# Optimization experiments

Measured on AMD Instinct MI355X. Metric: run time of the kernel, lower is better.

The kernel has to match this reference:

```python
import jax, jax.numpy as jnp
import numpy as np

N = 2_000_000
NUM_CLASSES = 64


def setup_inputs() -> dict:
    key = jax.random.key(0)
    k1, k2 = jax.random.split(key)
    # log-probability-like inputs (log_softmax so exp sums are well-scaled)
    logits = jax.random.normal(k1, (N, NUM_CLASSES), dtype=jnp.float32)
    predictions = jax.nn.log_softmax(logits, axis=-1)
    targets = jax.random.randint(k2, (N,), 0, NUM_CLASSES, dtype=jnp.int64)
    return {"predictions": predictions, "targets": targets}


def reference(predictions, targets):
    n = predictions.shape[0]
    num_classes = predictions.shape[1]
    # class_dist[i] = count of class i in targets  (create_distribution_tensor)
    ones = jnp.ones_like(targets, dtype=predictions.dtype)
    class_dist = jax.ops.segment_sum(ones, targets, num_segments=num_classes)
    # column sums of exp(predictions): sum_n exp(pred)[n, i]
    col_sum = jnp.sum(jnp.exp(predictions), axis=0)  # [C]
    penalty = jnp.sum((class_dist - col_sum) ** 2) / n
    # F.nll_loss with default mean reduction: -mean_n pred[n, targets[n]]
    picked = jnp.take_along_axis(predictions, targets[:, None], axis=1)[:, 0]
    nll = -jnp.mean(picked)
    return nll + penalty
```

## Files before the change

kernel.cpp:

```cpp
#include <hip/hip_runtime.h>

#define NUM_CLASSES 64
#define UNROLL 4
#define SLAB 16

typedef float f32x4 __attribute__((ext_vector_type(4)));

__global__ __launch_bounds__(256) void loss_pass1(
    const float* __restrict__ pred,
    const int* __restrict__ tgt,
    float* __restrict__ g_colsum,
    unsigned int* __restrict__ g_cnt,
    float* __restrict__ g_nll,
    int n)
{
    __shared__ float s_col[NUM_CLASSES];
    __shared__ unsigned int s_cnt[NUM_CLASSES];
    __shared__ float s_nll[4];

    const int t = threadIdx.x;
    if (t < NUM_CLASSES) { s_col[t] = 0.0f; s_cnt[t] = 0u; }
    __syncthreads();

    const int c16  = t & 15;
    const int rloc = t >> 4;
    const int c0   = c16 * 4;
    const int rows_per_block = SLAB * UNROLL;
    const long stride = (long)rows_per_block * gridDim.x;

    float ca0 = 0.f, ca1 = 0.f, ca2 = 0.f, ca3 = 0.f;
    float nllacc = 0.f;

    for (long base = (long)blockIdx.x * rows_per_block; base < n; base += stride) {
        f32x4 v[UNROLL];
        int   tg[UNROLL];

        if (base + rows_per_block <= n) {
            #pragma unroll
            for (int j = 0; j < UNROLL; ++j) {
                const long row = base + rloc + j * SLAB;
                v[j]  = __builtin_nontemporal_load(
                          reinterpret_cast<const f32x4*>(pred + row * NUM_CLASSES + c0));
                tg[j] = tgt[row];
            }
            #pragma unroll
            for (int j = 0; j < UNROLL; ++j) {
                ca0 += __expf(v[j][0]);
                ca1 += __expf(v[j][1]);
                ca2 += __expf(v[j][2]);
                ca3 += __expf(v[j][3]);
                if (c16 == j) atomicAdd(&s_cnt[tg[j]], 1u);
                const int d = tg[j] - c0;
                if ((unsigned)d < 4u) nllacc += v[j][d];
            }
        } else {
            #pragma unroll
            for (int j = 0; j < UNROLL; ++j) {
                const long row = base + rloc + j * SLAB;
                if (row >= n) continue;
                const f32x4 w = *reinterpret_cast<const f32x4*>(pred + row * NUM_CLASSES + c0);
                const int g = tgt[row];
                ca0 += __expf(w[0]);
                ca1 += __expf(w[1]);
                ca2 += __expf(w[2]);
                ca3 += __expf(w[3]);
                if (c16 == j) atomicAdd(&s_cnt[g], 1u);
                const int d = g - c0;
                if ((unsigned)d < 4u) nllacc += w[d];
            }
        }
    }

    atomicAdd(&s_col[c0 + 0], ca0);
    atomicAdd(&s_col[c0 + 1], ca1);
    atomicAdd(&s_col[c0 + 2], ca2);
    atomicAdd(&s_col[c0 + 3], ca3);

    for (int off = 32; off; off >>= 1) nllacc += __shfl_down(nllacc, off);
    if ((t & 63) == 0) s_nll[t >> 6] = nllacc;
    __syncthreads();

    if (t == 0) atomicAdd(g_nll, s_nll[0] + s_nll[1] + s_nll[2] + s_nll[3]);
    if (t < NUM_CLASSES) {
        atomicAdd(&g_colsum[t], s_col[t]);
        atomicAdd(&g_cnt[t], s_cnt[t]);
    }
}

__global__ void loss_finalize(const float* __restrict__ g_colsum,
                              const unsigned int* __restrict__ g_cnt,
                              const float* __restrict__ g_nll,
                              float* __restrict__ out, int n)
{
    const int t = threadIdx.x;
    const float diff = (float)g_cnt[t] - g_colsum[t];
    float p = diff * diff;
    for (int off = 32; off; off >>= 1) p += __shfl_down(p, off);
    if (t == 0) out[0] = (p - g_nll[0]) / (float)n;
}

extern "C" void kernel_launch(void* const* d_in, const int* in_sizes, int n_in,
                              void* d_out, int out_size, void* d_ws, size_t ws_size,
                              hipStream_t stream)
{
    const float* pred = (const float*)d_in[0];
    const int* tgt    = (const int*)d_in[1];
    const int n       = in_sizes[1];

    float*        g_colsum = (float*)d_ws;
    unsigned int* g_cnt    = (unsigned int*)((char*)d_ws + 256);
    float*        g_nll    = (float*)((char*)d_ws + 512);

    hipMemsetAsync(d_ws, 0, 1024, stream);

    loss_pass1<<<2048, 256, 0, stream>>>(pred, tgt, g_colsum, g_cnt, g_nll, n);
    loss_finalize<<<1, 64, 0, stream>>>(g_colsum, g_cnt, g_nll, (float*)d_out, n);
}
```

Measured before the change: 104.6 us.

## Replace global atomics and memset with per-block partials and parallel finalize

Each block now writes its per-class column sums, counts and NLL partial to a workspace slot instead of issuing global atomics, which also removes the hipMemsetAsync launch. A 1024-thread finalize kernel reduces the partials. Rows are split into contiguous per-block ranges rather than grid-strided slabs, and dynamic vector indexing is replaced by a select chain. This trades global atomic contention and a memset for extra workspace traffic and a heavier finalize.

```diff
diff --git a/kernel.cpp b/kernel.cpp
--- a/kernel.cpp
+++ b/kernel.cpp
@@ -1,73 +1,70 @@
 #include <hip/hip_runtime.h>
 
 #define NUM_CLASSES 64
-#define UNROLL 4
-#define SLAB 16
+#define MAX_GRID 2048
 
 typedef float f32x4 __attribute__((ext_vector_type(4)));
 
 __global__ __launch_bounds__(256) void loss_pass1(
     const float* __restrict__ pred,
     const int* __restrict__ tgt,
-    float* __restrict__ g_colsum,
-    unsigned int* __restrict__ g_cnt,
-    float* __restrict__ g_nll,
-    int n)
+    float* __restrict__ part_col,
+    float* __restrict__ part_cnt,
+    float* __restrict__ part_nll,
+    int n, int grid)
 {
     __shared__ float s_col[NUM_CLASSES];
     __shared__ unsigned int s_cnt[NUM_CLASSES];
     __shared__ float s_nll[4];
 
     const int t = threadIdx.x;
-    if (t < NUM_CLASSES) { s_col[t] = 0.0f; s_cnt[t] = 0u; }
+    if (t < NUM_CLASSES) { s_col[t] = 0.f; s_cnt[t] = 0u; }
     __syncthreads();
 
     const int c16  = t & 15;
     const int rloc = t >> 4;
     const int c0   = c16 * 4;
-    const int rows_per_block = SLAB * UNROLL;
-    const long stride = (long)rows_per_block * gridDim.x;
+
+    const long start = (long)blockIdx.x * n / grid;
+    const long end   = (long)(blockIdx.x + 1) * n / grid;
 
     float ca0 = 0.f, ca1 = 0.f, ca2 = 0.f, ca3 = 0.f;
     float nllacc = 0.f;
 
-    for (long base = (long)blockIdx.x * rows_per_block; base < n; base += stride) {
-        f32x4 v[UNROLL];
-        int   tg[UNROLL];
+    long base = start;
+    for (; base + 64 <= end; base += 64) {
+        f32x4 v[4];
+        int   tg[4];
+        #pragma unroll
+        for (int j = 0; j < 4; ++j) {
+            const long row = base + rloc + j * 16;
+            v[j]  = __builtin_nontemporal_load(
+                      reinterpret_cast<const f32x4*>(pred + row * NUM_CLASSES + c0));
+            tg[j] = tgt[row];
+        }
+        #pragma unroll
+        for (int j = 0; j < 4; ++j) {
+            ca0 += __expf(v[j][0]);
+            ca1 += __expf(v[j][1]);
+            ca2 += __expf(v[j][2]);
+            ca3 += __expf(v[j][3]);
+            if (c16 == j) atomicAdd(&s_cnt[tg[j]], 1u);
+            const int d = tg[j] - c0;
+            if ((unsigned)d < 4u)
+                nllacc += (d==0)?v[j][0]:(d==1)?v[j][1]:(d==2)?v[j][2]:v[j][3];
+        }
+    }
 
-        if (base + rows_per_block <= n) {
-            #pragma unroll
-            for (int j = 0; j < UNROLL; ++j) {
-                const long row = base + rloc + j * SLAB;
-                v[j]  = __builtin_nontemporal_load(
-                          reinterpret_cast<const f32x4*>(pred + row * NUM_CLASSES + c0));
-                tg[j] = tgt[row];
-            }
-            #pragma unroll
-            for (int j = 0; j < UNROLL; ++j) {
-                ca0 += __expf(v[j][0]);
-                ca1 += __expf(v[j][1]);
-                ca2 += __expf(v[j][2]);
-                ca3 += __expf(v[j][3]);
-                if (c16 == j) atomicAdd(&s_cnt[tg[j]], 1u);
-                const int d = tg[j] - c0;
-                if ((unsigned)d < 4u) nllacc += v[j][d];
-            }
-        } else {
-            #pragma unroll
-            for (int j = 0; j < UNROLL; ++j) {
-                const long row = base + rloc + j * SLAB;
-                if (row >= n) continue;
-                const f32x4 w = *reinterpret_cast<const f32x4*>(pred + row * NUM_CLASSES + c0);
-                const int g = tgt[row];
-                ca0 += __expf(w[0]);
-                ca1 += __expf(w[1]);
-                ca2 += __expf(w[2]);
-                ca3 += __expf(w[3]);
-                if (c16 == j) atomicAdd(&s_cnt[g], 1u);
-                const int d = g - c0;
-                if ((unsigned)d < 4u) nllacc += w[d];
-            }
+    #pragma unroll
+    for (int j = 0; j < 4; ++j) {
+        const long row = base + rloc + j * 16;
+        if (row < end) {
+            const f32x4 w = *reinterpret_cast<const f32x4*>(pred + row * NUM_CLASSES + c0);
+            const int g = tgt[row];
+            ca0 += __expf(w[0]); ca1 += __expf(w[1]); ca2 += __expf(w[2]); ca3 += __expf(w[3]);
+            if (c16 == j) atomicAdd(&s_cnt[g], 1u);
+            const int d = g - c0;
+            if ((unsigned)d < 4u) nllacc += (d==0)?w[0]:(d==1)?w[1]:(d==2)?w[2]:w[3];
         }
     }
 
@@ -80,23 +77,56 @@
     if ((t & 63) == 0) s_nll[t >> 6] = nllacc;
     __syncthreads();
 
-    if (t == 0) atomicAdd(g_nll, s_nll[0] + s_nll[1] + s_nll[2] + s_nll[3]);
     if (t < NUM_CLASSES) {
-        atomicAdd(&g_colsum[t], s_col[t]);
-        atomicAdd(&g_cnt[t], s_cnt[t]);
+        part_col[(long)blockIdx.x * NUM_CLASSES + t] = s_col[t];
+        part_cnt[(long)blockIdx.x * NUM_CLASSES + t] = (float)s_cnt[t];
     }
+    if (t == 0)
+        part_nll[blockIdx.x] = s_nll[0] + s_nll[1] + s_nll[2] + s_nll[3];
 }
 
-__global__ void loss_finalize(const float* __restrict__ g_colsum,
-                              const unsigned int* __restrict__ g_cnt,
-                              const float* __restrict__ g_nll,
-                              float* __restrict__ out, int n)
+__global__ __launch_bounds__(1024) void loss_finalize(
+    const float* __restrict__ part_col,
+    const float* __restrict__ part_cnt,
+    const float* __restrict__ part_nll,
+    float* __restrict__ out, int n, int grid)
 {
+    __shared__ float s_col[NUM_CLASSES];
+    __shared__ float s_cnt[NUM_CLASSES];
+    __shared__ float s_red[16];
+
     const int t = threadIdx.x;
-    const float diff = (float)g_cnt[t] - g_colsum[t];
-    float p = diff * diff;
-    for (int off = 32; off; off >>= 1) p += __shfl_down(p, off);
-    if (t == 0) out[0] = (p - g_nll[0]) / (float)n;
+    if (t < NUM_CLASSES) { s_col[t] = 0.f; s_cnt[t] = 0.f; }
+    __syncthreads();
+
+    const int c   = t & 63;
+    const int grp = t >> 6;
+
+    float sc = 0.f, sn = 0.f;
+    for (int b = grp; b < grid; b += 16) {
+        sc += part_col[(long)b * NUM_CLASSES + c];
+        sn += part_cnt[(long)b * NUM_CLASSES + c];
+    }
+    atomicAdd(&s_col[c], sc);
+    atomicAdd(&s_cnt[c], sn);
+
+    float np = 0.f;
+    for (int b = t; b < grid; b += 1024) np += part_nll[b];
+    for (int off = 32; off; off >>= 1) np += __shfl_down(np, off);
+    if ((t & 63) == 0) s_red[t >> 6] = np;
+    __syncthreads();
+
+    if (t < NUM_CLASSES) {
+        const float diff = s_cnt[t] - s_col[t];
+        float p = diff * diff;
+        for (int off = 32; off; off >>= 1) p += __shfl_down(p, off);
+        if (t == 0) {
+            float nll = 0.f;
+            #pragma unroll
+            for (int i = 0; i < 16; ++i) nll += s_red[i];
+            out[0] = (p - nll) / (float)n;
+        }
+    }
 }
 
 extern "C" void kernel_launch(void* const* d_in, const int* in_sizes, int n_in,
@@ -107,12 +137,17 @@
     const int* tgt    = (const int*)d_in[1];
     const int n       = in_sizes[1];
 
-    float*        g_colsum = (float*)d_ws;
-    unsigned int* g_cnt    = (unsigned int*)((char*)d_ws + 256);
-    float*        g_nll    = (float*)((char*)d_ws + 512);
+    int grid = MAX_GRID;
+    const size_t per_block = (size_t)NUM_CLASSES * 4 * 2 + 4;
+    if (ws_size < (size_t)grid * per_block) {
+        grid = (int)(ws_size / per_block);
+        if (grid < 1) grid = 1;
+    }
 
-    hipMemsetAsync(d_ws, 0, 1024, stream);
+    float* part_col = (float*)d_ws;
+    float* part_cnt = part_col + (size_t)grid * NUM_CLASSES;
+    float* part_nll = part_cnt + (size_t)grid * NUM_CLASSES;
 
-    loss_pass1<<<2048, 256, 0, stream>>>(pred, tgt, g_colsum, g_cnt, g_nll, n);
-    loss_finalize<<<1, 64, 0, stream>>>(g_colsum, g_cnt, g_nll, (float*)d_out, n);
+    loss_pass1<<<grid, 256, 0, stream>>>(pred, tgt, part_col, part_cnt, part_nll, n, grid);
+    loss_finalize<<<1, 1024, 0, stream>>>(part_col, part_cnt, part_nll, (float*)d_out, n, grid);
 }
```

After: 121.4 us. 1.16x slower.
